# Optimization experiments

Hardware: AMD Instinct MI355X
Metric: run time of the kernel (lower is better)

Reference implementation:

```python
import jax, jax.numpy as jnp
import numpy as np

B, S, DIN, D, H, DOUT, W = 4, 2048, 256, 512, 8, 128, 64
HD = D // H


def setup_inputs() -> dict:
    key = jax.random.key(0)
    ks = jax.random.split(key, 16)
    r = lambda k, shape, s=0.02: (jax.random.normal(k, shape, jnp.float32) * s)
    return dict(
        x=jax.random.normal(ks[0], (B, S, DIN), jnp.float32),
        pos=jax.random.normal(ks[1], (1, S, D), jnp.float32),  # torch.randn init
        win_w=r(ks[2], (DIN, D)), win_b=jnp.zeros((D,), jnp.float32),
        l_wqkv=r(ks[3], (3, D, D)), l_bqkv=jnp.zeros((3, D), jnp.float32),
        l_wo=r(ks[4], (D, D)), l_bo=jnp.zeros((D,), jnp.float32),
        g_wqkv=r(ks[5], (3, D, D)), g_bqkv=jnp.zeros((3, D), jnp.float32),
        g_wo=r(ks[6], (D, D)), g_bo=jnp.zeros((D,), jnp.float32),
        gate_w=r(ks[7], (2 * D, D)), gate_b=jnp.zeros((D,), jnp.float32),
        ffn_w1=r(ks[8], (D, 2 * D)), ffn_b1=jnp.zeros((2 * D,), jnp.float32),
        ffn_w2=r(ks[9], (2 * D, D)), ffn_b2=jnp.zeros((D,), jnp.float32),
        n1_g=jnp.ones((D,), jnp.float32), n1_b=jnp.zeros((D,), jnp.float32),
        n2_g=jnp.ones((D,), jnp.float32), n2_b=jnp.zeros((D,), jnp.float32),
        n3_g=jnp.ones((D,), jnp.float32), n3_b=jnp.zeros((D,), jnp.float32),
        out_w=r(ks[10], (D, DOUT)), out_b=jnp.zeros((DOUT,), jnp.float32),
    )


def _ln(x, g, b, eps=1e-5):
    m = x.mean(-1, keepdims=True)
    v = ((x - m) ** 2).mean(-1, keepdims=True)
    return (x - m) * jax.lax.rsqrt(v + eps) * g + b


def _mha(x, wqkv, bqkv, wo, bo, mask):
    b, s, d = x.shape
    q = (x @ wqkv[0] + bqkv[0]).reshape(b, s, H, HD)
    k = (x @ wqkv[1] + bqkv[1]).reshape(b, s, H, HD)
    v = (x @ wqkv[2] + bqkv[2]).reshape(b, s, H, HD)
    scores = jnp.einsum('bqhd,bkhd->bhqk', q, k) / np.sqrt(HD).astype(np.float32)
    if mask is not None:
        scores = scores + mask  # additive -inf band mask
    attn = jax.nn.softmax(scores, axis=-1)
    o = jnp.einsum('bhqk,bkhd->bqhd', attn, v).reshape(b, s, d)
    return o @ wo + bo


def reference(x, pos, win_w, win_b,
              l_wqkv, l_bqkv, l_wo, l_bo,
              g_wqkv, g_bqkv, g_wo, g_bo,
              gate_w, gate_b, ffn_w1, ffn_b1, ffn_w2, ffn_b2,
              n1_g, n1_b, n2_g, n2_b, n3_g, n3_b, out_w, out_b):
    s = x.shape[1]
    # band mask: row i allows cols [i - W//2, i + W//2] (matches create_local_mask)
    idx = jnp.arange(s)
    band = jnp.abs(idx[:, None] - idx[None, :]) <= (W // 2)
    mask = jnp.where(band, 0.0, -jnp.inf).astype(jnp.float32)

    h = x @ win_w + win_b + pos
    local_out = _mha(h, l_wqkv, l_bqkv, l_wo, l_bo, mask)
    global_out = _mha(h, g_wqkv, g_bqkv, g_wo, g_bo, None)

    combined = jnp.concatenate([local_out, global_out], axis=-1)
    gate = jnp.tanh(jax.nn.relu(combined @ gate_w + gate_b))
    fused = gate * local_out + (1.0 - gate) * global_out

    h = _ln(h + fused, n1_g, n1_b)
    ffn = jax.nn.relu(h @ ffn_w1 + ffn_b1) @ ffn_w2 + ffn_b2
    h = _ln(h + ffn, n2_g, n2_b)
    h = _ln(h, n3_g, n3_b)
    pooled = h.mean(axis=1)  # AdaptiveAvgPool1d(1) over seq
    return pooled @ out_w + out_b
```

## Files before the change

kernel.cpp:

```cpp
#include <hip/hip_runtime.h>
#include <math.h>
#include <stdint.h>

#define S_LEN 2048
#define DMODEL 512
#define NHEAD 8
#define BATCH 4
#define M_ROWS (BATCH * S_LEN)
#define UAC 4194304

typedef __attribute__((ext_vector_type(8))) short frag8;
typedef __attribute__((ext_vector_type(4))) float f32x4;

__device__ inline unsigned short f2bf(float f) {
    unsigned int u = __float_as_uint(f);
    return (unsigned short)((u + 0x7FFFu + ((u >> 16) & 1u)) >> 16);
}
__device__ inline float bf2f(unsigned short h) {
    return __uint_as_float(((unsigned int)h) << 16);
}

#if __has_builtin(__builtin_amdgcn_exp2f)
#define EXP2(x) __builtin_amdgcn_exp2f(x)
#else
#define EXP2(x) __expf(0.6931471805599453f * (x))
#endif

#if __has_builtin(__builtin_amdgcn_global_load_lds)
__device__ __forceinline__ void glds16(const void* g, void* l, int lane) {
    __builtin_amdgcn_global_load_lds(
        (__attribute__((address_space(1))) void*)(uintptr_t)g,
        (__attribute__((address_space(3))) void*)(uintptr_t)l, 16, 0, 0);
    (void)lane;
}
#else
__device__ __forceinline__ void glds16(const void* g, void* l, int lane) {
    ((uint4*)l)[lane] = ((const uint4*)g)[0];
}
#endif

struct WSeg { const float* src; unsigned short* dst; int K; int N; int start; };
struct WTab { WSeg s[12]; };

__global__ __launch_bounds__(256) void wcast_all(WTab tab)
{
    __shared__ float t[32][33];
    const int bid = blockIdx.x;
    int si = 0;
#pragma unroll
    for (int i = 1; i < 12; ++i) if (bid >= tab.s[i].start) si = i;
    const WSeg sg = tab.s[si];
    const int tile = bid - sg.start;
    const int nk = sg.K >> 5;
    const int k0 = (tile % nk) * 32, n0 = (tile / nk) * 32;
    {
        int kk = threadIdx.x >> 3, nq = (threadIdx.x & 7) * 4;
        float4 v = *(const float4*)&sg.src[(size_t)(k0 + kk) * sg.N + n0 + nq];
        t[kk][nq + 0] = v.x; t[kk][nq + 1] = v.y; t[kk][nq + 2] = v.z; t[kk][nq + 3] = v.w;
    }
    __syncthreads();
    {
        int n = threadIdx.x >> 3, kq = (threadIdx.x & 7) * 4;
        ushort4 o;
        o.x = f2bf(t[kq + 0][n]); o.y = f2bf(t[kq + 1][n]);
        o.z = f2bf(t[kq + 2][n]); o.w = f2bf(t[kq + 3][n]);
        *(ushort4*)&sg.dst[(size_t)(n0 + n) * sg.K + k0 + kq] = o;
    }
}

__global__ __launch_bounds__(256) void castx_kernel(
    const float* __restrict__ x, unsigned short* __restrict__ xb)
{
    const size_t i = ((size_t)blockIdx.x * 256 + threadIdx.x) * 8;
    float4 a = *(const float4*)&x[i], b = *(const float4*)&x[i + 4];
    unsigned short us[8];
    us[0] = f2bf(a.x); us[1] = f2bf(a.y); us[2] = f2bf(a.z); us[3] = f2bf(a.w);
    us[4] = f2bf(b.x); us[5] = f2bf(b.y); us[6] = f2bf(b.z); us[7] = f2bf(b.w);
    *(uint4*)&xb[i] = *(uint4*)us;
}

__global__ __launch_bounds__(256) void vtrans_kernel(
    const unsigned short* __restrict__ V, unsigned short* __restrict__ Vt)
{
    __shared__ unsigned short T[64][72];
    const int st = blockIdx.x, bh = blockIdx.y;
    const int b = bh >> 3, h = bh & 7;
    const int tid = threadIdx.x;
    {
        const int s = tid >> 2, d0 = (tid & 3) * 16;
        const unsigned short* src = V + ((size_t)(b * S_LEN + st * 64 + s) * DMODEL + h * 64 + d0);
        *(uint4*)&T[s][d0] = *(const uint4*)src;
        *(uint4*)&T[s][d0 + 8] = *(const uint4*)(src + 8);
    }
    __syncthreads();
    {
        const int d = tid >> 2, s0 = (tid & 3) * 16;
        unsigned short buf[16];
#pragma unroll
        for (int j = 0; j < 16; ++j) buf[j] = T[s0 + j][d];
        unsigned short* dst = Vt + ((size_t)(bh * 64 + d) * S_LEN + st * 64 + s0);
        *(uint4*)&dst[0] = *(const uint4*)&buf[0];
        *(uint4*)&dst[8] = *(const uint4*)&buf[8];
    }
}

template <int MODE, int BN>
__global__ __launch_bounds__(256) void gemm_mfma(
    const unsigned short* __restrict__ A, const unsigned short* __restrict__ A2,
    const unsigned short* __restrict__ Wt, const float* __restrict__ bias,
    const float* __restrict__ bias2, const float* __restrict__ pos,
    unsigned short* __restrict__ C, unsigned short* __restrict__ C2,
    int M, int N, int K)
{
    constexpr int UN = BN / 32;
    __shared__ unsigned short As[128 * 64];
    __shared__ unsigned short Bs[BN * 64];
    const int tid = threadIdx.x;
    const int wave = tid >> 6, lane = tid & 63;
    const int lr = lane & 15, quad = lane >> 4;
    const int bm = blockIdx.x * 128, bn = blockIdx.y * BN;
    const int rm = (wave >> 1) * 64, rn = (wave & 1) * (BN / 2);
    const int Khalf = K >> 1;
    const int KA = (MODE == 3) ? Khalf : K;

    const unsigned short* SA = A;
    const unsigned short* SW = Wt;
    const float* SBIAS = bias;
    unsigned short* SC = C;
    if constexpr (MODE == 6) {
        if (blockIdx.z) { SA = A2; SW = Wt + 512 * 512; SBIAS = bias2; SC = C2; }
    }

    const int lrow = lane >> 3;
    const int gch = ((lane & 7) - lrow) & 7;
    const size_t laneA = (size_t)(bm + wave * 32 + lrow) * KA + gch * 8;
    const size_t laneB = (size_t)(bn + wave * (BN / 4) + lrow) * K + gch * 8;
    unsigned short* ldsA = As + wave * 2048;
    unsigned short* ldsB = Bs + wave * (BN * 16);

    f32x4 acc[4][UN];
#pragma unroll
    for (int t = 0; t < 4; ++t)
#pragma unroll
        for (int u = 0; u < UN; ++u) acc[t][u] = (f32x4){0.f, 0.f, 0.f, 0.f};

    const int sw0 = ((quad + lr) & 7) * 8;
    const int sw1 = ((quad + lr + 4) & 7) * 8;

    for (int k0 = 0; k0 < K; k0 += 64) {
        __syncthreads();
        const unsigned short* Ab; int kadj;
        if constexpr (MODE == 3) { Ab = (k0 < Khalf) ? A : A2; kadj = k0 & (Khalf - 1); }
        else { Ab = SA; kadj = k0; }
        const unsigned short* pa = Ab + laneA + kadj;
        glds16(pa,           ldsA,        lane);
        glds16(pa + 8 * KA,  ldsA + 512,  lane);
        glds16(pa + 16 * KA, ldsA + 1024, lane);
        glds16(pa + 24 * KA, ldsA + 1536, lane);
        const unsigned short* pb = SW + laneB + k0;
#pragma unroll
        for (int i = 0; i < UN; ++i)
            glds16(pb + i * 8 * K, ldsB + i * 512, lane);
        __syncthreads();

#pragma unroll
        for (int kc = 0; kc < 2; ++kc) {
            const int sw = kc ? sw1 : sw0;
            frag8 af[4], bf[UN];
#pragma unroll
            for (int t = 0; t < 4; ++t)
                af[t] = *(const frag8*)&As[(rm + t * 16 + lr) * 64 + sw];
#pragma unroll
            for (int u = 0; u < UN; ++u)
                bf[u] = *(const frag8*)&Bs[(rn + u * 16 + lr) * 64 + sw];
#pragma unroll
            for (int t = 0; t < 4; ++t)
#pragma unroll
                for (int u = 0; u < UN; ++u)
                    acc[t][u] = __builtin_amdgcn_mfma_f32_16x16x32_bf16(
                        af[t], bf[u], acc[t][u], 0, 0, 0);
        }
    }

#pragma unroll
    for (int t = 0; t < 4; ++t) {
#pragma unroll
        for (int i = 0; i < 4; ++i) {
            const int m = bm + rm + t * 16 + quad * 4 + i;
#pragma unroll
            for (int u = 0; u < UN; ++u) {
                const int n = bn + rn + u * 16 + lr;
                if constexpr (MODE == 5) {
                    const int mat = n >> 9;
                    const int nn = n & 511;
                    const float* bp = (mat < 3) ? (bias + (mat << 9))
                                                : (bias2 + ((mat - 3) << 9));
                    float v = acc[t][u][i] + bp[nn];
                    if (mat == 0 || mat == 3) v *= 0.18033688011112042f;
                    C[(size_t)mat * UAC + (size_t)m * DMODEL + nn] = f2bf(v);
                } else {
                    float v = acc[t][u][i] + SBIAS[n];
                    if constexpr (MODE == 1) v += pos[(size_t)(m & (S_LEN - 1)) * N + n];
                    if constexpr (MODE == 2) v = fmaxf(v, 0.0f);
                    if constexpr (MODE == 3) {
                        float g = tanhf(fmaxf(v, 0.0f));
                        float lo = bf2f(A[(size_t)m * Khalf + n]);
                        float go = bf2f(A2[(size_t)m * Khalf + n]);
                        v = g * lo + (1.0f - g) * go;
                    }
                    SC[(size_t)m * N + n] = f2bf(v);
                }
            }
        }
    }
}

#define ISSUE_KV(KT, BUF) do {                                                  \
    const unsigned short* _kp = kbase + (size_t)(KT) * (64 * DMODEL);           \
    const unsigned short* _vp = vbase + (size_t)(KT) * 64;                      \
    unsigned short* _lk = Ks + (BUF) * 4096 + wave * 1024;                      \
    unsigned short* _lv = Vts + (BUF) * 4096 + wave * 1024;                     \
    glds16(_kp, _lk, lane); glds16(_kp + 8 * DMODEL, _lk + 512, lane);          \
    glds16(_vp, _lv, lane); glds16(_vp + 8 * S_LEN, _lv + 512, lane);           \
} while (0)

__global__ __launch_bounds__(256) void attn_mfma(
    const unsigned short* __restrict__ Q, const unsigned short* __restrict__ Kv,
    const unsigned short* __restrict__ Vt, unsigned short* __restrict__ O, int masked)
{
    __shared__ unsigned short Ks[2 * 64 * 64];
    __shared__ unsigned short Vts[2 * 64 * 64];
    __shared__ unsigned short Ps[64 * 64];
    const int qt = blockIdx.x, h = blockIdx.y, b = blockIdx.z;
    const int tid = threadIdx.x;
    const int wave = tid >> 6, lane = tid & 63;
    const int lr = lane & 15, quad = lane >> 4;

    {
        const int q = tid >> 2, c8 = (tid & 3) * 2;
        const unsigned short* src = Q + ((size_t)(b * S_LEN + qt * 64 + q) * DMODEL + h * 64 + c8 * 8);
        *(uint4*)&Ps[q * 64 + (((c8 + q) & 7) * 8)] = *(const uint4*)src;
        *(uint4*)&Ps[q * 64 + (((c8 + 1 + q) & 7) * 8)] = *(const uint4*)(src + 8);
    }
    const int sw0 = ((quad + lr) & 7) * 8;
    const int sw1 = ((quad + lr + 4) & 7) * 8;
    const int prow = (wave * 16 + lr) * 64;
    frag8 qf[2];
    qf[0] = *(const frag8*)&Ps[prow + sw0];
    qf[1] = *(const frag8*)&Ps[prow + sw1];

    f32x4 oacc[4];
#pragma unroll
    for (int t = 0; t < 4; ++t) oacc[t] = (f32x4){0.f, 0.f, 0.f, 0.f};
    float l_r = 0.f;

    int kt0 = 0, kt1 = S_LEN / 64 - 1;
    if (masked) { kt0 = qt > 0 ? qt - 1 : 0; kt1 = qt < 31 ? qt + 1 : 31; }
    const int nt = kt1 - kt0 + 1;

    const int lrow = lane >> 3;
    const int gch = ((lane & 7) - lrow) & 7;
    const unsigned short* kbase = Kv + ((size_t)(b * S_LEN + kt0 * 64 + wave * 16 + lrow) * DMODEL + h * 64 + gch * 8);
    const unsigned short* vbase = Vt + ((size_t)((b * 8 + h) * 64 + wave * 16 + lrow) * S_LEN + kt0 * 64 + gch * 8);

    ISSUE_KV(0, 0);

    for (int it = 0; it < nt; ++it) {
        const int buf = it & 1;
        __syncthreads();
        if (it + 1 < nt) ISSUE_KV(it + 1, buf ^ 1);

        const unsigned short* kb = Ks + buf * 4096;
        const unsigned short* vb = Vts + buf * 4096;

        f32x4 sacc[4];
#pragma unroll
        for (int t = 0; t < 4; ++t) sacc[t] = (f32x4){0.f, 0.f, 0.f, 0.f};
#pragma unroll
        for (int kc = 0; kc < 2; ++kc) {
            const int sw = kc ? sw1 : sw0;
#pragma unroll
            for (int t = 0; t < 4; ++t) {
                frag8 kf = *(const frag8*)&kb[(t * 16 + lr) * 64 + sw];
                sacc[t] = __builtin_amdgcn_mfma_f32_16x16x32_bf16(kf, qf[kc], sacc[t], 0, 0, 0);
            }
        }

        const int kt = kt0 + it;
#pragma unroll
        for (int t = 0; t < 4; ++t) {
            float p0 = EXP2(sacc[t][0]);
            float p1 = EXP2(sacc[t][1]);
            float p2 = EXP2(sacc[t][2]);
            float p3 = EXP2(sacc[t][3]);
            if (masked) {
                const int qa = qt * 64 + wave * 16 + lr;
                const int ca = kt * 64 + t * 16 + quad * 4;
                int d0 = qa - ca;
                if (d0 > 32 || d0 < -32) p0 = 0.f;
                int d1 = qa - (ca + 1);
                if (d1 > 32 || d1 < -32) p1 = 0.f;
                int d2 = qa - (ca + 2);
                if (d2 > 32 || d2 < -32) p2 = 0.f;
                int d3 = qa - (ca + 3);
                if (d3 > 32 || d3 < -32) p3 = 0.f;
            }
            const unsigned u0 = __float_as_uint(p0) & 0xFFFF0000u;
            const unsigned u1 = __float_as_uint(p1) & 0xFFFF0000u;
            const unsigned u2 = __float_as_uint(p2) & 0xFFFF0000u;
            const unsigned u3 = __float_as_uint(p3) & 0xFFFF0000u;
            l_r += (__uint_as_float(u0) + __uint_as_float(u1)) +
                   (__uint_as_float(u2) + __uint_as_float(u3));
            uint2 pw;
            pw.x = __builtin_amdgcn_perm(u1, u0, 0x07060302);
            pw.y = __builtin_amdgcn_perm(u3, u2, 0x07060302);
            const int slot = ((2 * t + (quad >> 1) + lr) & 7) * 8 + (quad & 1) * 4;
            *(uint2*)&Ps[prow + slot] = pw;
        }

#pragma unroll
        for (int cc = 0; cc < 2; ++cc) {
            const int sw = cc ? sw1 : sw0;
            frag8 pa = *(const frag8*)&Ps[prow + sw];
#pragma unroll
            for (int t = 0; t < 4; ++t) {
                frag8 vf = *(const frag8*)&vb[(t * 16 + lr) * 64 + sw];
                oacc[t] = __builtin_amdgcn_mfma_f32_16x16x32_bf16(pa, vf, oacc[t], 0, 0, 0);
            }
        }
    }

    l_r += __shfl_xor(l_r, 16);
    l_r += __shfl_xor(l_r, 32);
#pragma unroll
    for (int i = 0; i < 4; ++i) {
        const float inv = 1.0f / __shfl(l_r, quad * 4 + i);
        const int q = qt * 64 + wave * 16 + quad * 4 + i;
#pragma unroll
        for (int t = 0; t < 4; ++t)
            O[(size_t)(b * S_LEN + q) * DMODEL + h * 64 + t * 16 + lr] = f2bf(oacc[t][i] * inv);
    }
}

__device__ inline float wave_sum64(float v) {
#pragma unroll
    for (int off = 1; off < 64; off <<= 1) v += __shfl_xor(v, off);
    return v;
}

__global__ __launch_bounds__(256) void ln_res_kernel(
    const unsigned short* __restrict__ A, const unsigned short* __restrict__ Bb,
    const float* __restrict__ g, const float* __restrict__ be,
    unsigned short* __restrict__ out)
{
    const size_t row = blockIdx.x * 4 + (threadIdx.x >> 6);
    const int lane = threadIdx.x & 63;
    float x[8]; float s = 0.f;
#pragma unroll
    for (int k = 0; k < 8; ++k) {
        size_t idx = row * DMODEL + k * 64 + lane;
        x[k] = bf2f(A[idx]) + bf2f(Bb[idx]);
        s += x[k];
    }
    s = wave_sum64(s);
    float mean = s * (1.0f / DMODEL);
    float v = 0.f;
#pragma unroll
    for (int k = 0; k < 8; ++k) { float d = x[k] - mean; v += d * d; }
    v = wave_sum64(v) * (1.0f / DMODEL);
    float r = rsqrtf(v + 1e-5f);
#pragma unroll
    for (int k = 0; k < 8; ++k)
        out[row * DMODEL + k * 64 + lane] =
            f2bf((x[k] - mean) * r * g[k * 64 + lane] + be[k * 64 + lane]);
}

__global__ __launch_bounds__(256) void ln_double_kernel(
    const unsigned short* __restrict__ A, const unsigned short* __restrict__ Bb,
    const float* __restrict__ g2, const float* __restrict__ b2,
    const float* __restrict__ g3, const float* __restrict__ b3,
    unsigned short* __restrict__ out)
{
    const size_t row = blockIdx.x * 4 + (threadIdx.x >> 6);
    const int lane = threadIdx.x & 63;
    float x[8]; float s = 0.f;
#pragma unroll
    for (int k = 0; k < 8; ++k) {
        size_t idx = row * DMODEL + k * 64 + lane;
        x[k] = bf2f(A[idx]) + bf2f(Bb[idx]);
        s += x[k];
    }
    s = wave_sum64(s);
    float mean = s * (1.0f / DMODEL);
    float v = 0.f;
#pragma unroll
    for (int k = 0; k < 8; ++k) { float d = x[k] - mean; v += d * d; }
    v = wave_sum64(v) * (1.0f / DMODEL);
    float r = rsqrtf(v + 1e-5f);
    float t[8]; float s2 = 0.f;
#pragma unroll
    for (int k = 0; k < 8; ++k) {
        t[k] = (x[k] - mean) * r * g2[k * 64 + lane] + b2[k * 64 + lane];
        s2 += t[k];
    }
    s2 = wave_sum64(s2);
    float mean2 = s2 * (1.0f / DMODEL);
    float v2 = 0.f;
#pragma unroll
    for (int k = 0; k < 8; ++k) { float d = t[k] - mean2; v2 += d * d; }
    v2 = wave_sum64(v2) * (1.0f / DMODEL);
    float r2 = rsqrtf(v2 + 1e-5f);
#pragma unroll
    for (int k = 0; k < 8; ++k)
        out[row * DMODEL + k * 64 + lane] =
            f2bf((t[k] - mean2) * r2 * g3[k * 64 + lane] + b3[k * 64 + lane]);
}

__global__ __launch_bounds__(256) void pool_kernel(
    const unsigned short* __restrict__ h2, float* __restrict__ pooled)
{
    const int b = blockIdx.x >> 4;
    const int chunk = blockIdx.x & 15;
    const int tid = threadIdx.x;
    float s0 = 0.f, s1 = 0.f;
    size_t base = (size_t)(b * S_LEN + chunk * 128) * DMODEL;
    for (int r = 0; r < 128; ++r) {
        s0 += bf2f(h2[base + (size_t)r * DMODEL + tid]);
        s1 += bf2f(h2[base + (size_t)r * DMODEL + 256 + tid]);
    }
    atomicAdd(&pooled[b * DMODEL + tid], s0);
    atomicAdd(&pooled[b * DMODEL + 256 + tid], s1);
}

__global__ __launch_bounds__(128) void out_kernel(
    const float* __restrict__ pooled, const float* __restrict__ w,
    const float* __restrict__ bias, float* __restrict__ out)
{
    const int b = blockIdx.x;
    const int o = threadIdx.x;
    float acc = 0.f;
    for (int d = 0; d < DMODEL; ++d)
        acc += pooled[b * DMODEL + d] * w[d * 128 + o];
    out[b * 128 + o] = acc * (1.0f / S_LEN) + bias[o];
}

extern "C" void kernel_launch(void* const* d_in, const int* in_sizes, int n_in,
                              void* d_out, int out_size, void* d_ws, size_t ws_size,
                              hipStream_t stream)
{
    const float* x      = (const float*)d_in[0];
    const float* pos    = (const float*)d_in[1];
    const float* win_w  = (const float*)d_in[2];
    const float* win_b  = (const float*)d_in[3];
    const float* l_wqkv = (const float*)d_in[4];
    const float* l_bqkv = (const float*)d_in[5];
    const float* l_wo   = (const float*)d_in[6];
    const float* l_bo   = (const float*)d_in[7];
    const float* g_wqkv = (const float*)d_in[8];
    const float* g_bqkv = (const float*)d_in[9];
    const float* g_wo   = (const float*)d_in[10];
    const float* g_bo   = (const float*)d_in[11];
    const float* gate_w = (const float*)d_in[12];
    const float* gate_b = (const float*)d_in[13];
    const float* ffn_w1 = (const float*)d_in[14];
    const float* ffn_b1 = (const float*)d_in[15];
    const float* ffn_w2 = (const float*)d_in[16];
    const float* ffn_b2 = (const float*)d_in[17];
    const float* n1_g   = (const float*)d_in[18];
    const float* n1_b   = (const float*)d_in[19];
    const float* n2_g   = (const float*)d_in[20];
    const float* n2_b   = (const float*)d_in[21];
    const float* n3_g   = (const float*)d_in[22];
    const float* n3_b   = (const float*)d_in[23];
    const float* out_w  = (const float*)d_in[24];
    const float* out_b  = (const float*)d_in[25];
    float* out = (float*)d_out;

    unsigned short* ws16 = (unsigned short*)d_ws;
    const size_t UA = (size_t)UAC;
    unsigned short* H    = ws16 + 0 * UA;
    unsigned short* QKV  = ws16 + 1 * UA;
    unsigned short* Ql   = ws16 + 1 * UA;
    unsigned short* Kl   = ws16 + 2 * UA;
    unsigned short* Vl   = ws16 + 3 * UA;
    unsigned short* Qg   = ws16 + 4 * UA;
    unsigned short* Kg   = ws16 + 5 * UA;
    unsigned short* Vg   = ws16 + 6 * UA;
    unsigned short* VT   = ws16 + 7 * UA;
    unsigned short* AOl    = Vl;
    unsigned short* AOg    = Ql;
    unsigned short* LO     = Kl;
    unsigned short* GO     = Qg;
    unsigned short* FUSED  = Kg;
    unsigned short* H1     = Vg;
    unsigned short* FFNMID = Vl;
    unsigned short* FFNOUT = Ql;
    unsigned short* H2     = Kl;
    float* POOLED = (float*)(void*)H;

    unsigned short* wt = ws16 + 8 * UA;
    unsigned short* win_t  = wt;
    unsigned short* lqkv_t = win_t  + 131072;
    unsigned short* gqkv_t = lqkv_t + 786432;
    unsigned short* lwo_t  = gqkv_t + 786432;
    unsigned short* gwo_t  = lwo_t  + 262144;
    unsigned short* gate_t = gwo_t  + 262144;
    unsigned short* ffn1_t = gate_t + 524288;
    unsigned short* ffn2_t = ffn1_t + 524288;
    unsigned short* xb     = ffn2_t + 524288;

    WTab tab;
    tab.s[0]  = {win_w,             win_t,             256,  512,    0};
    tab.s[1]  = {l_wqkv + 0*262144, lqkv_t + 0*262144, 512,  512,  128};
    tab.s[2]  = {l_wqkv + 1*262144, lqkv_t + 1*262144, 512,  512,  384};
    tab.s[3]  = {l_wqkv + 2*262144, lqkv_t + 2*262144, 512,  512,  640};
    tab.s[4]  = {g_wqkv + 0*262144, gqkv_t + 0*262144, 512,  512,  896};
    tab.s[5]  = {g_wqkv + 1*262144, gqkv_t + 1*262144, 512,  512, 1152};
    tab.s[6]  = {g_wqkv + 2*262144, gqkv_t + 2*262144, 512,  512, 1408};
    tab.s[7]  = {l_wo,              lwo_t,             512,  512, 1664};
    tab.s[8]  = {g_wo,              gwo_t,             512,  512, 1920};
    tab.s[9]  = {gate_w,            gate_t,            1024, 512, 2176};
    tab.s[10] = {ffn_w1,            ffn1_t,            512, 1024, 2688};
    tab.s[11] = {ffn_w2,            ffn2_t,            1024, 512, 3200};

    dim3 blk(256);
    wcast_all<<<dim3(3712), blk, 0, stream>>>(tab);
    castx_kernel<<<dim3(1024), blk, 0, stream>>>(x, xb);

    dim3 gD(M_ROWS / 128, 512 / 64);
    dim3 gW(M_ROWS / 128, 512 / 64, 2);
    dim3 gQ(M_ROWS / 128, 3072 / 128);
    dim3 gF(M_ROWS / 128, 1024 / 128);
    dim3 gA(S_LEN / 64, NHEAD, BATCH);
    dim3 gV(S_LEN / 64, BATCH * NHEAD);

    gemm_mfma<1, 64><<<gD, blk, 0, stream>>>(xb, nullptr, win_t, win_b, nullptr, pos, H, nullptr, M_ROWS, 512, 256);

    gemm_mfma<5, 128><<<gQ, blk, 0, stream>>>(H, nullptr, lqkv_t, l_bqkv, g_bqkv, nullptr, QKV, nullptr, M_ROWS, 3072, 512);

    vtrans_kernel<<<gV, blk, 0, stream>>>(Vl, VT);
    attn_mfma<<<gA, blk, 0, stream>>>(Ql, Kl, VT, AOl, 1);
    vtrans_kernel<<<gV, blk, 0, stream>>>(Vg, VT);
    attn_mfma<<<gA, blk, 0, stream>>>(Qg, Kg, VT, AOg, 0);

    gemm_mfma<6, 64><<<gW, blk, 0, stream>>>(AOl, AOg, lwo_t, l_bo, g_bo, nullptr, LO, GO, M_ROWS, 512, 512);

    gemm_mfma<3, 64><<<gD, blk, 0, stream>>>(LO, GO, gate_t, gate_b, nullptr, nullptr, FUSED, nullptr, M_ROWS, 512, 1024);

    ln_res_kernel<<<M_ROWS / 4, blk, 0, stream>>>(H, FUSED, n1_g, n1_b, H1);

    gemm_mfma<2, 128><<<gF, blk, 0, stream>>>(H1, nullptr, ffn1_t, ffn_b1, nullptr, nullptr, FFNMID, nullptr, M_ROWS, 1024, 512);
    gemm_mfma<0, 64><<<gD, blk, 0, stream>>>(FFNMID, nullptr, ffn2_t, ffn_b2, nullptr, nullptr, FFNOUT, nullptr, M_ROWS, 512, 1024);

    ln_double_kernel<<<M_ROWS / 4, blk, 0, stream>>>(H1, FFNOUT, n2_g, n2_b, n3_g, n3_b, H2);

    hipMemsetAsync(POOLED, 0, BATCH * DMODEL * sizeof(float), stream);
    pool_kernel<<<dim3(BATCH * 16), blk, 0, stream>>>(H2, POOLED);
    out_kernel<<<dim3(BATCH), dim3(128), 0, stream>>>(POOLED, out_w, out_b, out);
}
```

Baseline: 358.6 us.

## Split global attention across two KV halves, merge vtrans launches, drop double buffering

Global attention is split along the key dimension into two halves, each handled by a separate block that writes unnormalized partial outputs and row sums. A new combine kernel adds the halves and normalizes. The two V-transpose launches are merged into one with a z dimension, and the KV double-buffered prefetch is replaced by a single-buffered load with two barriers per tile. This doubles the number of global attention blocks for better occupancy, at the cost of extra memory traffic, an extra launch, and lost load/compute overlap. Partial outputs are rounded to bf16 before combining, which adds some rounding error.

```diff
diff --git a/kernel.cpp b/kernel.cpp
--- a/kernel.cpp
+++ b/kernel.cpp
@@ -79,10 +79,13 @@
     *(uint4*)&xb[i] = *(uint4*)us;
 }
 
-__global__ __launch_bounds__(256) void vtrans_kernel(
-    const unsigned short* __restrict__ V, unsigned short* __restrict__ Vt)
+__global__ __launch_bounds__(256) void vtrans2_kernel(
+    const unsigned short* __restrict__ Vl, const unsigned short* __restrict__ Vg,
+    unsigned short* __restrict__ VTl, unsigned short* __restrict__ VTg)
 {
     __shared__ unsigned short T[64][72];
+    const unsigned short* V = blockIdx.z ? Vg : Vl;
+    unsigned short* Vt = blockIdx.z ? VTg : VTl;
     const int st = blockIdx.x, bh = blockIdx.y;
     const int b = bh >> 3, h = bh & 7;
     const int tid = threadIdx.x;
@@ -215,23 +218,18 @@
     }
 }
 
-#define ISSUE_KV(KT, BUF) do {                                                  \
-    const unsigned short* _kp = kbase + (size_t)(KT) * (64 * DMODEL);           \
-    const unsigned short* _vp = vbase + (size_t)(KT) * 64;                      \
-    unsigned short* _lk = Ks + (BUF) * 4096 + wave * 1024;                      \
-    unsigned short* _lv = Vts + (BUF) * 4096 + wave * 1024;                     \
-    glds16(_kp, _lk, lane); glds16(_kp + 8 * DMODEL, _lk + 512, lane);          \
-    glds16(_vp, _lv, lane); glds16(_vp + 8 * S_LEN, _lv + 512, lane);           \
-} while (0)
-
 __global__ __launch_bounds__(256) void attn_mfma(
     const unsigned short* __restrict__ Q, const unsigned short* __restrict__ Kv,
-    const unsigned short* __restrict__ Vt, unsigned short* __restrict__ O, int masked)
-{
-    __shared__ unsigned short Ks[2 * 64 * 64];
-    __shared__ unsigned short Vts[2 * 64 * 64];
+    const unsigned short* __restrict__ Vt, unsigned short* __restrict__ O,
+    unsigned short* __restrict__ O2, float* __restrict__ Lp,
+    int masked, int split)
+{
+    __shared__ unsigned short Ks[64 * 64];
+    __shared__ unsigned short Vts[64 * 64];
     __shared__ unsigned short Ps[64 * 64];
-    const int qt = blockIdx.x, h = blockIdx.y, b = blockIdx.z;
+    const int qt = blockIdx.x, h = blockIdx.y;
+    const int b = split ? (int)(blockIdx.z >> 1) : (int)blockIdx.z;
+    const int half = split ? (int)(blockIdx.z & 1) : 0;
     const int tid = threadIdx.x;
     const int wave = tid >> 6, lane = tid & 63;
     const int lr = lane & 15, quad = lane >> 4;
@@ -254,24 +252,26 @@
     for (int t = 0; t < 4; ++t) oacc[t] = (f32x4){0.f, 0.f, 0.f, 0.f};
     float l_r = 0.f;
 
-    int kt0 = 0, kt1 = S_LEN / 64 - 1;
-    if (masked) { kt0 = qt > 0 ? qt - 1 : 0; kt1 = qt < 31 ? qt + 1 : 31; }
-    const int nt = kt1 - kt0 + 1;
+    int kt0, kt1;
+    if (split) { kt0 = half * 16; kt1 = kt0 + 15; }
+    else if (masked) { kt0 = qt > 0 ? qt - 1 : 0; kt1 = qt < 31 ? qt + 1 : 31; }
+    else { kt0 = 0; kt1 = 31; }
 
     const int lrow = lane >> 3;
     const int gch = ((lane & 7) - lrow) & 7;
-    const unsigned short* kbase = Kv + ((size_t)(b * S_LEN + kt0 * 64 + wave * 16 + lrow) * DMODEL + h * 64 + gch * 8);
-    const unsigned short* vbase = Vt + ((size_t)((b * 8 + h) * 64 + wave * 16 + lrow) * S_LEN + kt0 * 64 + gch * 8);
-
-    ISSUE_KV(0, 0);
-
-    for (int it = 0; it < nt; ++it) {
-        const int buf = it & 1;
+    const unsigned short* kp = Kv + ((size_t)(b * S_LEN + kt0 * 64 + wave * 16 + lrow) * DMODEL + h * 64 + gch * 8);
+    const unsigned short* vp = Vt + ((size_t)((b * 8 + h) * 64 + wave * 16 + lrow) * S_LEN + kt0 * 64 + gch * 8);
+    unsigned short* lk = Ks + wave * 1024;
+    unsigned short* lv = Vts + wave * 1024;
+
+    for (int kt = kt0; kt <= kt1; ++kt) {
         __syncthreads();
-        if (it + 1 < nt) ISSUE_KV(it + 1, buf ^ 1);
-
-        const unsigned short* kb = Ks + buf * 4096;
-        const unsigned short* vb = Vts + buf * 4096;
+        glds16(kp, lk, lane);
+        glds16(kp + 8 * DMODEL, lk + 512, lane);
+        glds16(vp, lv, lane);
+        glds16(vp + 8 * S_LEN, lv + 512, lane);
+        kp += 64 * DMODEL; vp += 64;
+        __syncthreads();
 
         f32x4 sacc[4];
 #pragma unroll
@@ -281,12 +281,11 @@
             const int sw = kc ? sw1 : sw0;
 #pragma unroll
             for (int t = 0; t < 4; ++t) {
-                frag8 kf = *(const frag8*)&kb[(t * 16 + lr) * 64 + sw];
+                frag8 kf = *(const frag8*)&Ks[(t * 16 + lr) * 64 + sw];
                 sacc[t] = __builtin_amdgcn_mfma_f32_16x16x32_bf16(kf, qf[kc], sacc[t], 0, 0, 0);
             }
         }
 
-        const int kt = kt0 + it;
 #pragma unroll
         for (int t = 0; t < 4; ++t) {
             float p0 = EXP2(sacc[t][0]);
@@ -324,7 +323,7 @@
             frag8 pa = *(const frag8*)&Ps[prow + sw];
 #pragma unroll
             for (int t = 0; t < 4; ++t) {
-                frag8 vf = *(const frag8*)&vb[(t * 16 + lr) * 64 + sw];
+                frag8 vf = *(const frag8*)&Vts[(t * 16 + lr) * 64 + sw];
                 oacc[t] = __builtin_amdgcn_mfma_f32_16x16x32_bf16(pa, vf, oacc[t], 0, 0, 0);
             }
         }
@@ -332,14 +331,50 @@
 
     l_r += __shfl_xor(l_r, 16);
     l_r += __shfl_xor(l_r, 32);
-#pragma unroll
-    for (int i = 0; i < 4; ++i) {
-        const float inv = 1.0f / __shfl(l_r, quad * 4 + i);
-        const int q = qt * 64 + wave * 16 + quad * 4 + i;
-#pragma unroll
-        for (int t = 0; t < 4; ++t)
-            O[(size_t)(b * S_LEN + q) * DMODEL + h * 64 + t * 16 + lr] = f2bf(oacc[t][i] * inv);
-    }
+    if (split) {
+        if (lane < 16)
+            Lp[((half * 4 + b) * 8 + h) * 2048 + qt * 64 + wave * 16 + lane] = l_r;
+        unsigned short* dst = half ? O2 : O;
+#pragma unroll
+        for (int i = 0; i < 4; ++i) {
+            const int q = qt * 64 + wave * 16 + quad * 4 + i;
+#pragma unroll
+            for (int t = 0; t < 4; ++t)
+                dst[(size_t)(b * S_LEN + q) * DMODEL + h * 64 + t * 16 + lr] = f2bf(oacc[t][i]);
+        }
+    } else {
+#pragma unroll
+        for (int i = 0; i < 4; ++i) {
+            const float inv = 1.0f / __shfl(l_r, quad * 4 + i);
+            const int q = qt * 64 + wave * 16 + quad * 4 + i;
+#pragma unroll
+            for (int t = 0; t < 4; ++t)
+                O[(size_t)(b * S_LEN + q) * DMODEL + h * 64 + t * 16 + lr] = f2bf(oacc[t][i] * inv);
+        }
+    }
+}
+
+__global__ __launch_bounds__(256) void combine_kernel(
+    unsigned short* __restrict__ P0, const unsigned short* __restrict__ P1,
+    const float* __restrict__ Lp)
+{
+    const size_t e = ((size_t)blockIdx.x * 256 + threadIdx.x) * 8;
+    const int b = (int)(e >> 20);
+    const int rem = (int)(e & 1048575);
+    const int q = rem >> 9;
+    const int h = (rem & 511) >> 6;
+    const int lidx = (b * 8 + h) * 2048 + q;
+    const float inv = 1.0f / (Lp[lidx] + Lp[65536 + lidx]);
+    uint4 a = *(uint4*)&P0[e];
+    uint4 c = *(const uint4*)&P1[e];
+    unsigned short o[8];
+#define CMB(wa, wc, j) { \
+    float a0 = __uint_as_float((wa) << 16), a1 = __uint_as_float((wa) & 0xFFFF0000u); \
+    float c0 = __uint_as_float((wc) << 16), c1 = __uint_as_float((wc) & 0xFFFF0000u); \
+    o[j] = f2bf((a0 + c0) * inv); o[(j) + 1] = f2bf((a1 + c1) * inv); }
+    CMB(a.x, c.x, 0) CMB(a.y, c.y, 2) CMB(a.z, c.z, 4) CMB(a.w, c.w, 6)
+#undef CMB
+    *(uint4*)&P0[e] = *(uint4*)o;
 }
 
 __device__ inline float wave_sum64(float v) {
@@ -486,7 +521,7 @@
     unsigned short* Qg   = ws16 + 4 * UA;
     unsigned short* Kg   = ws16 + 5 * UA;
     unsigned short* Vg   = ws16 + 6 * UA;
-    unsigned short* VT   = ws16 + 7 * UA;
+    unsigned short* VTl  = ws16 + 7 * UA;
     unsigned short* AOl    = Vl;
     unsigned short* AOg    = Ql;
     unsigned short* LO     = Kl;
@@ -508,6 +543,9 @@
     unsigned short* ffn1_t = gate_t + 524288;
     unsigned short* ffn2_t = ffn1_t + 524288;
     unsigned short* xb     = ffn2_t + 524288;
+    unsigned short* VTg    = xb + 2097152;
+    unsigned short* PO1    = VTg + UA;
+    float*          Lp     = (float*)(void*)(PO1 + UA);
 
     WTab tab;
     tab.s[0]  = {win_w,             win_t,             256,  512,    0};
@@ -524,24 +562,26 @@
     tab.s[11] = {ffn_w2,            ffn2_t,            1024, 512, 3200};
 
     dim3 blk(256);
+    castx_kernel<<<dim3(1024), blk, 0, stream>>>(x, xb);
     wcast_all<<<dim3(3712), blk, 0, stream>>>(tab);
-    castx_kernel<<<dim3(1024), blk, 0, stream>>>(x, xb);
 
     dim3 gD(M_ROWS / 128, 512 / 64);
     dim3 gW(M_ROWS / 128, 512 / 64, 2);
     dim3 gQ(M_ROWS / 128, 3072 / 128);
     dim3 gF(M_ROWS / 128, 1024 / 128);
-    dim3 gA(S_LEN / 64, NHEAD, BATCH);
-    dim3 gV(S_LEN / 64, BATCH * NHEAD);
+    dim3 gAL(S_LEN / 64, NHEAD, BATCH);
+    dim3 gAG(S_LEN / 64, NHEAD, BATCH*2);
+    dim3 gV(S_LEN / 64, BATCH * NHEAD, 2);
 
     gemm_mfma<1, 64><<<gD, blk, 0, stream>>>(xb, nullptr, win_t, win_b, nullptr, pos, H, nullptr, M_ROWS, 512, 256);
 
     gemm_mfma<5, 128><<<gQ, blk, 0, stream>>>(H, nullptr, lqkv_t, l_bqkv, g_bqkv, nullptr, QKV, nullptr, M_ROWS, 3072, 512);
 
-    vtrans_kernel<<<gV, blk, 0, stream>>>(Vl, VT);
-    attn_mfma<<<gA, blk, 0, stream>>>(Ql, Kl, VT, AOl, 1);
-    vtrans_kernel<<<gV, blk, 0, stream>>>(Vg, VT);
-    attn_mfma<<<gA, blk, 0, stream>>>(Qg, Kg, VT, AOg, 0);
+    vtrans2_kernel<<<gV, blk, 0, stream>>>(Vl, Vg, VTl, VTg);
+
+    attn_mfma<<<gAL, blk, 0, stream>>>(Ql, Kl, VTl, AOl, nullptr, nullptr, 1, 0);
+    attn_mfma<<<gAG, blk, 0, stream>>>(Qg, Kg, VTg, AOg, PO1, Lp, 0, 1);
+    combine_kernel<<<dim3(2048), blk, 0, stream>>>(AOg, PO1, Lp);
 
     gemm_mfma<6, 64><<<gW, blk, 0, stream>>>(AOl, AOg, lwo_t, l_bo, g_bo, nullptr, LO, GO, M_ROWS, 512, 512);
 
```

Result: slower. 367.9 us (+2.6%).
